# Optimization experiments

Hardware: AMD Instinct MI355X
Metric: run time of the kernel (lower is better)

## Reference

```python
import jax, jax.numpy as jnp
import numpy as np


def _cas(N, dtype=jnp.float32):
    # cas(2*pi*k*n/N) = cos + sin, symmetric NxN matrix (rebuilt per call, as in the original)
    n = jnp.arange(N, dtype=dtype)
    ang = (2.0 * jnp.pi / N) * jnp.outer(n, n)
    return jnp.cos(ang) + jnp.sin(ang)


def dht(x):
    # Discrete Hartley transform over the last axis via dense matmul
    return x @ _cas(x.shape[-1], x.dtype)


def reverse(x):
    # X[(N - k) mod N]: index 0 stays, rest are flipped
    return jnp.roll(jnp.flip(x, axis=-1), 1, axis=-1)


def setup_inputs() -> dict:
    key = jax.random.key(0)
    k1, k2 = jax.random.split(key)
    B, Cin, Cout, N, M = 4, 16, 16, 8192, 64
    x = jax.random.normal(k1, (B, Cin, N), dtype=jnp.float32)
    scale = 1.0 / (Cin * Cout)
    weights1 = scale * jax.random.uniform(k2, (Cin, Cout, M), dtype=jnp.float32)
    return {"x": x, "weights1": weights1}


def reference(x, weights1):
    B, Cin, N = x.shape
    Cout, M = weights1.shape[1], weights1.shape[2]
    N2 = N // 2 + 1

    # DHT of the input over the spatial axis
    x_ht = dht(x)                                   # [B, Cin, N]

    # compl_mul1d on the first `modes1` Hartley coefficients
    hp = dht(x_ht[:, :, :M])                        # [B, Cin, M] (DHT applied again, as in source)
    hq = dht(weights1)                              # [Cin, Cout, M]
    rp = reverse(hp)
    rq = reverse(hq)
    # (t1 + t2 + t3 - t4)/2 == ((hp+rp)@hq + (hp-rp)@rq)/2
    hz = 0.5 * (jnp.einsum('bix,iox->box', hp + rp, hq)
                + jnp.einsum('bix,iox->box', hp - rp, rq))  # [B, Cout, M]
    # idht normalizes by the TOTAL element count of its argument (quirk preserved)
    z = dht(hz) / (B * Cout * M)                    # [B, Cout, M]

    # Scatter into half-spectrum buffer, then idht (imag part is always zero -> stay real)
    out_ht = jnp.zeros((B, Cout, N2), dtype=x.dtype).at[:, :, :M].set(z)
    out = dht(out_ht) / (B * Cout * N2)             # [B, Cout, N//2 + 1]
    return out
```

## Files before the change

kernel.cpp:

```cpp
#include <hip/hip_runtime.h>
#include <math.h>

#define TWO_PI 6.283185307179586f

__global__ __launch_bounds__(256) void kA(const float* __restrict__ x,
                                          const float* __restrict__ w1,
                                          float* __restrict__ P,
                                          float* __restrict__ hq) {
  __shared__ float rows[4][64];
  __shared__ float cas64[64];
  const int blk = blockIdx.x;
  const int t = threadIdx.x;

  if (blk < 256) {
    const int r  = blk & 63;
    const int mb = (blk >> 6) & 1;
    const int nh = (blk >> 7) & 1;
    const int l  = t & 63;
    const int w  = t >> 6;
    const int mbase = mb * 32 + w * 8;
    const float* xr = x + r * 8192 + nh * 4096;

    const float step = TWO_PI / 8192.0f;
    float u[8], v[8], Cs[8], Ss[8];
    float accA[8][4];
    float accB[8][3];

#pragma unroll
    for (int q = 0; q < 8; ++q) {
      const int m = mbase + q;
      const int idx0 = ((nh * 4096 + 4 * l) * m) & 8191;
      float s0, c0;
      __sincosf((float)idx0 * step, &s0, &c0);
      u[q] = c0 + s0;
      v[q] = c0 - s0;
      const int idxs = (256 * m) & 8191;
      float ss, cs;
      __sincosf((float)idxs * step, &ss, &cs);
      Cs[q] = cs;
      Ss[q] = ss;
#pragma unroll
      for (int j = 0; j < 4; ++j) accA[q][j] = 0.0f;
#pragma unroll
      for (int j = 0; j < 3; ++j) accB[q][j] = 0.0f;
    }

#pragma unroll 8
    for (int it = 0; it < 16; ++it) {
      const float4 xv = *reinterpret_cast<const float4*>(xr + it * 256 + 4 * l);
#pragma unroll
      for (int q = 0; q < 8; ++q) {
        accA[q][0] += xv.x * u[q];
        accA[q][1] += xv.y * u[q];
        accA[q][2] += xv.z * u[q];
        accA[q][3] += xv.w * u[q];
        accB[q][0] += xv.y * v[q];
        accB[q][1] += xv.z * v[q];
        accB[q][2] += xv.w * v[q];
        const float un = Cs[q] * u[q] + Ss[q] * v[q];
        const float vn = Cs[q] * v[q] - Ss[q] * u[q];
        u[q] = un;
        v[q] = vn;
      }
    }

#pragma unroll
    for (int q = 0; q < 8; ++q) {
      const int m = mbase + q;
      const float d = (float)m * step;
      float acc = accA[q][0];
#pragma unroll
      for (int j = 1; j < 4; ++j) {
        float sj, cj;
        __sincosf((float)j * d, &sj, &cj);
        acc += cj * accA[q][j] + sj * accB[q][j - 1];
      }
#pragma unroll
      for (int off = 32; off > 0; off >>= 1) acc += __shfl_xor(acc, off, 64);
      if (l == q) P[(r * 64 + m) * 2 + nh] = acc;
    }
  } else {
    const int sub = t >> 6;
    const int c = t & 63;
    if (t < 64) {
      float s, cc;
      __sincosf((float)t * (TWO_PI / 64.0f), &s, &cc);
      cas64[t] = cc + s;
    }
    const int b2 = blk - 256;
    rows[sub][c] = w1[(b2 * 4 + sub) * 64 + c];
    __syncthreads();
    float acc = 0.0f;
#pragma unroll 8
    for (int m = 0; m < 64; ++m) acc += rows[sub][m] * cas64[(m * c) & 63];
    hq[(b2 * 4 + sub) * 64 + c] = acc;
  }
}

__global__ __launch_bounds__(256) void kB(const float* __restrict__ P,
                                          const float* __restrict__ hq,
                                          float* __restrict__ z) {
  const int blk = blockIdx.x;
  const int b = blk >> 4;
  const int o = blk & 15;
  __shared__ float sAT[64][20];
  __shared__ float sq[16][64];
  __shared__ float hp[16][64];
  __shared__ float hz[64];
  __shared__ float red[4][64];
  __shared__ float cas64[64];
  const int t = threadIdx.x;
  const int m = t & 63;
  const int sub = t >> 6;

  if (t < 64) {
    float s, cc;
    __sincosf((float)t * (TWO_PI / 64.0f), &s, &cc);
    cas64[t] = cc + s;
  }
  for (int idx = t; idx < 1024; idx += 256) {
    const int i = idx >> 6;
    const int c = idx & 63;
    const float2 pv =
        *reinterpret_cast<const float2*>(&P[(((b * 16 + i) << 6) + c) * 2]);
    sAT[c][i] = pv.x + pv.y;
    sq[i][c] = hq[(((i * 16 + o) << 6)) + c];
  }
  __syncthreads();

  {
    float sd, cd;
    __sincosf((float)m * (TWO_PI / 64.0f), &sd, &cd);
    float u = 1.0f, v = 1.0f;
    float acc0 = 0.0f, acc1 = 0.0f, acc2 = 0.0f, acc3 = 0.0f;
#pragma unroll 8
    for (int c = 0; c < 64; ++c) {
      const float4 av = *reinterpret_cast<const float4*>(&sAT[c][sub * 4]);
      acc0 += av.x * u;
      acc1 += av.y * u;
      acc2 += av.z * u;
      acc3 += av.w * u;
      const float un = cd * u + sd * v;
      const float vn = cd * v - sd * u;
      u = un;
      v = vn;
    }
    hp[sub * 4 + 0][m] = acc0;
    hp[sub * 4 + 1][m] = acc1;
    hp[sub * 4 + 2][m] = acc2;
    hp[sub * 4 + 3][m] = acc3;
  }
  __syncthreads();

  const int mr = (64 - m) & 63;
  float a = 0.0f;
#pragma unroll
  for (int ii = 0; ii < 4; ++ii) {
    const int i = sub * 4 + ii;
    const float p  = hp[i][m];
    const float pr = hp[i][mr];
    const float qq = sq[i][m];
    const float qr = sq[i][mr];
    a += 0.5f * ((p + pr) * qq + (p - pr) * qr);
  }
  red[sub][m] = a;
  __syncthreads();
  if (t < 64) hz[t] = red[0][t] + red[1][t] + red[2][t] + red[3][t];
  __syncthreads();

  float zz = 0.0f;
#pragma unroll
  for (int jj = 0; jj < 16; ++jj) {
    const int mm = sub * 16 + jj;
    zz += hz[mm] * cas64[(mm * m) & 63];
  }
  red[sub][m] = zz;
  __syncthreads();
  if (t < 64)
    z[blk * 64 + t] =
        (red[0][t] + red[1][t] + red[2][t] + red[3][t]) * (1.0f / 4096.0f);
}

__global__ __launch_bounds__(256) void kC(const float* __restrict__ z,
                                          float* __restrict__ out) {
  const int row = blockIdx.x;
  const int kc  = blockIdx.y;
  __shared__ float zr[64];
  const int t = threadIdx.x;
  if (t < 64) zr[t] = z[row * 64 + t];
  __syncthreads();
  const int k = kc * 256 + t;
  if (k >= 4097) return;
  const float d = (float)k * (TWO_PI / 4097.0f);
  float sd, cd;
  __sincosf(d, &sd, &cd);
  float u = 1.0f, v = 1.0f;
  float acc = 0.0f;
#pragma unroll 8
  for (int m = 0; m < 64; ++m) {
    acc += zr[m] * u;
    const float un = cd * u + sd * v;
    const float vn = cd * v - sd * u;
    u = un;
    v = vn;
  }
  out[row * 4097 + k] = acc * (1.0f / 262208.0f);
}

extern "C" void kernel_launch(void* const* d_in, const int* in_sizes, int n_in,
                              void* d_out, int out_size, void* d_ws, size_t ws_size,
                              hipStream_t stream) {
  const float* x  = (const float*)d_in[0];
  const float* w1 = (const float*)d_in[1];
  float* out = (float*)d_out;
  float* ws = (float*)d_ws;
  float* P  = ws;
  float* hq = ws + 8192;
  float* z  = ws + 24576;

  kA<<<320, 256, 0, stream>>>(x, w1, P, hq);
  kB<<<64, 256, 0, stream>>>(P, hq, z);
  kC<<<dim3(64, 17), 256, 0, stream>>>(z, out);
}
```

Measured before the change: 74.61 us.

## Replace sincos calls with shared twiddle tables and split recurrences

In kA, per-lane __sincosf calls are replaced by coarse/fine sine-cosine tables in shared memory combined with the angle-addition formula. The final per-j twiddles are computed once per lane and broadcast with shuffles. In kC, the serial 64-step rotation recurrence is split into 8 independent accumulator pairs that advance by an 8-step rotation and are combined with precomputed base twiddles at the end. This removes transcendental work and shortens the dependency chain, at the cost of an extra syncthreads, more registers, and slightly different rounding.

```diff
diff --git a/kernel.cpp b/kernel.cpp
--- a/kernel.cpp
+++ b/kernel.cpp
@@ -7,12 +7,27 @@
                                           const float* __restrict__ w1,
                                           float* __restrict__ P,
                                           float* __restrict__ hq) {
+  __shared__ float sH[128], cH[128], sL[64], cL[64];
   __shared__ float rows[4][64];
   __shared__ float cas64[64];
   const int blk = blockIdx.x;
   const int t = threadIdx.x;
 
   if (blk < 256) {
+    if (t < 128) {
+      float s, c;
+      __sincosf((float)t * (TWO_PI / 128.0f), &s, &c);
+      sH[t] = s;
+      cH[t] = c;
+    } else if (t < 192) {
+      const int g = t - 128;
+      float s, c;
+      __sincosf((float)g * (TWO_PI / 8192.0f), &s, &c);
+      sL[g] = s;
+      cL[g] = c;
+    }
+    __syncthreads();
+
     const int r  = blk & 63;
     const int mb = (blk >> 6) & 1;
     const int nh = (blk >> 7) & 1;
@@ -21,7 +36,6 @@
     const int mbase = mb * 32 + w * 8;
     const float* xr = x + r * 8192 + nh * 4096;
 
-    const float step = TWO_PI / 8192.0f;
     float u[8], v[8], Cs[8], Ss[8];
     float accA[8][4];
     float accB[8][3];
@@ -30,15 +44,14 @@
     for (int q = 0; q < 8; ++q) {
       const int m = mbase + q;
       const int idx0 = ((nh * 4096 + 4 * l) * m) & 8191;
-      float s0, c0;
-      __sincosf((float)idx0 * step, &s0, &c0);
+      const int h = idx0 >> 6, g = idx0 & 63;
+      const float c0 = cH[h] * cL[g] - sH[h] * sL[g];
+      const float s0 = sH[h] * cL[g] + cH[h] * sL[g];
       u[q] = c0 + s0;
       v[q] = c0 - s0;
-      const int idxs = (256 * m) & 8191;
-      float ss, cs;
-      __sincosf((float)idxs * step, &ss, &cs);
-      Cs[q] = cs;
-      Ss[q] = ss;
+      const int ih = (4 * m) & 127;
+      Cs[q] = cH[ih];
+      Ss[q] = sH[ih];
 #pragma unroll
       for (int j = 0; j < 4; ++j) accA[q][j] = 0.0f;
 #pragma unroll
@@ -64,20 +77,28 @@
       }
     }
 
+    float cval, sval;
+    {
+      const int qq = (l >> 2) & 7;
+      const int jj = l & 3;
+      const int jm = jj * (mbase + qq);
+      const int h = jm >> 6, g = jm & 63;
+      cval = cH[h] * cL[g] - sH[h] * sL[g];
+      sval = sH[h] * cL[g] + cH[h] * sL[g];
+    }
+
 #pragma unroll
     for (int q = 0; q < 8; ++q) {
-      const int m = mbase + q;
-      const float d = (float)m * step;
       float acc = accA[q][0];
 #pragma unroll
       for (int j = 1; j < 4; ++j) {
-        float sj, cj;
-        __sincosf((float)j * d, &sj, &cj);
+        const float cj = __shfl(cval, q * 4 + j, 64);
+        const float sj = __shfl(sval, q * 4 + j, 64);
         acc += cj * accA[q][j] + sj * accB[q][j - 1];
       }
 #pragma unroll
       for (int off = 32; off > 0; off >>= 1) acc += __shfl_xor(acc, off, 64);
-      if (l == q) P[(r * 64 + m) * 2 + nh] = acc;
+      if (l == q) P[(r * 64 + (mbase + q)) * 2 + nh] = acc;
     }
   } else {
     const int sub = t >> 6;
@@ -191,19 +212,41 @@
   __syncthreads();
   const int k = kc * 256 + t;
   if (k >= 4097) return;
-  const float d = (float)k * (TWO_PI / 4097.0f);
-  float sd, cd;
-  __sincosf(d, &sd, &cd);
+  const float th = (float)k * (TWO_PI / 4097.0f);
+  float s1, c1;
+  __sincosf(th, &s1, &c1);
+
+  float cw[8], sw[8];
+  cw[0] = 1.0f; sw[0] = 0.0f;
+  cw[1] = c1;   sw[1] = s1;
+#pragma unroll
+  for (int b = 2; b < 8; ++b) {
+    cw[b] = cw[b - 1] * c1 - sw[b - 1] * s1;
+    sw[b] = sw[b - 1] * c1 + cw[b - 1] * s1;
+  }
+  const float c8 = cw[7] * c1 - sw[7] * s1;
+  const float s8 = sw[7] * c1 + cw[7] * s1;
+
+  float A[8], B[8];
+#pragma unroll
+  for (int b = 0; b < 8; ++b) { A[b] = 0.0f; B[b] = 0.0f; }
   float u = 1.0f, v = 1.0f;
-  float acc = 0.0f;
-#pragma unroll 8
-  for (int m = 0; m < 64; ++m) {
-    acc += zr[m] * u;
-    const float un = cd * u + sd * v;
-    const float vn = cd * v - sd * u;
+#pragma unroll
+  for (int a = 0; a < 8; ++a) {
+#pragma unroll
+    for (int b = 0; b < 8; ++b) {
+      const float zz = zr[a * 8 + b];
+      A[b] += zz * u;
+      B[b] += zz * v;
+    }
+    const float un = c8 * u + s8 * v;
+    const float vn = c8 * v - s8 * u;
     u = un;
     v = vn;
   }
+  float acc = 0.0f;
+#pragma unroll
+  for (int b = 0; b < 8; ++b) acc += cw[b] * A[b] + sw[b] * B[b];
   out[row * 4097 + k] = acc * (1.0f / 262208.0f);
 }
 
```

Measured after the change: 72.19 us. 3.2% less time.
